# Optimization experiments

Measured on AMD Instinct MI355X. Metric: run time of the kernel, lower is better.

## Reference

```python
import jax, jax.numpy as jnp
import numpy as np

N_HEAD = 12


def build_mask(T, N):
    """Boolean mask, True = blocked. Mirrors st_mask construction for
    text_mask_mode='none', domain_present=None, text_to_motion_attn=False."""
    L = 3 * T + 5 * N
    r = jnp.arange(T)
    causal = r[:, None] >= r[None, :]          # allowed (lower-tri incl diag)
    strict = r[:, None] > r[None, :]           # allowed (strictly lower)
    m = jnp.zeros((L, L), dtype=bool)
    ml = 3 * T
    # motion-motion region starts fully blocked, then 7 sub-blocks opened
    m = m.at[:ml, :ml].set(True)
    m = m.at[0:T, 0:T].set(~causal)
    m = m.at[T:2 * T, 0:T].set(~causal)
    m = m.at[T:2 * T, T:2 * T].set(~strict)
    m = m.at[T:2 * T, 2 * T:3 * T].set(~strict)
    m = m.at[2 * T:3 * T, 0:T].set(~causal)
    m = m.at[2 * T:3 * T, T:2 * T].set(~causal)
    m = m.at[2 * T:3 * T, 2 * T:3 * T].set(~strict)
    # motion queries -> text keys: blocked by default
    m = m.at[:ml, ml:].set(True)
    # text queries -> motion keys: blocked (text_to_motion_attn=False)
    m = m.at[ml:, :ml].set(True)
    # text_mask_mode='none': up/down motion rows attend ALL text domains
    m = m.at[T:3 * T, ml:].set(False)
    return m


def setup_inputs() -> dict:
    key = jax.random.key(0)
    ks = jax.random.split(key, 9)
    C = 768
    B, T, N = 4, 512, 16
    L = 3 * T + 5 * N
    s = 1.0 / np.sqrt(C)
    return {
        "x": jax.random.normal(ks[0], (B, L, C), dtype=jnp.float32),
        "Wq": jax.random.normal(ks[1], (C, C), dtype=jnp.float32) * s,
        "bq": jax.random.normal(ks[2], (C,), dtype=jnp.float32) * 0.02,
        "Wk": jax.random.normal(ks[3], (C, C), dtype=jnp.float32) * s,
        "bk": jax.random.normal(ks[4], (C,), dtype=jnp.float32) * 0.02,
        "Wv": jax.random.normal(ks[5], (C, C), dtype=jnp.float32) * s,
        "bv": jax.random.normal(ks[6], (C,), dtype=jnp.float32) * 0.02,
        "Wp": jax.random.normal(ks[7], (C, C), dtype=jnp.float32) * s,
        "bp": jax.random.normal(ks[8], (C,), dtype=jnp.float32) * 0.02,
        "T_motion": 512,
        "N": 16,
    }


def reference(x, Wq, bq, Wk, bk, Wv, bv, Wp, bp, T_motion, N):
    B, L, C = x.shape
    nh = N_HEAD
    hd = C // nh
    # projections (torch Linear: x @ W.T + b)
    q = (x @ Wq.T + bq).reshape(B, L, nh, hd).transpose(0, 2, 1, 3)
    k = (x @ Wk.T + bk).reshape(B, L, nh, hd).transpose(0, 2, 1, 3)
    v = (x @ Wv.T + bv).reshape(B, L, nh, hd).transpose(0, 2, 1, 3)
    att = jnp.einsum('bhqd,bhkd->bhqk', q, k) * (1.0 / np.sqrt(hd))
    mask = build_mask(T_motion, N)                 # [L, L], True = blocked
    att = jnp.where(mask[None, None], -jnp.inf, att)
    att = jax.nn.softmax(att, axis=-1)
    y = jnp.einsum('bhqk,bhkd->bhqd', att, v)      # [B, nh, L, hd]
    y = y.transpose(0, 2, 1, 3).reshape(B, L, C)
    return y @ Wp.T + bp
```

## Files before the change

### kernel.cpp

```cpp
#include <hip/hip_runtime.h>

typedef _Float16 half8_t __attribute__((ext_vector_type(8)));
typedef _Float16 half4_t __attribute__((ext_vector_type(4)));
typedef int      int2_t  __attribute__((ext_vector_type(2)));
typedef float    f32x4   __attribute__((ext_vector_type(4)));

#define L_TOT 1616
#define L_PAD 1664
#define ML    1536
#define TT    512
#define CDIM  768
#define HD    64
#define NH    12
#define MTOT  6464

#define QK_SCALE 0.1803368801f
#define FIXED_M 10.0f

#if __has_builtin(__builtin_amdgcn_exp2f)
#define EXP2F(x) __builtin_amdgcn_exp2f(x)
#else
#define EXP2F(x) __expf((x) * 0.69314718056f)
#endif

typedef __attribute__((address_space(3))) void  as3_void;
typedef const __attribute__((address_space(1))) void as1_void;
__device__ __forceinline__ void gload_lds16(const void* g, void* l) {
  __builtin_amdgcn_global_load_lds((as1_void*)g, (as3_void*)l, 16, 0, 0);
}

__device__ __forceinline__ bool is_blocked(int i, int j) {
  if (j >= L_TOT) return true;
  if (i >= ML) return j < ML;
  if (j >= ML) return i < TT;
  int bi = i >> 9, bj = j >> 9;
  int a = i & 511, c = j & 511;
  if (bi == 0) return !(bj == 0 && c <= a);
  if (bi == 1) {
    if (bj == 0) return !(c <= a);
    return !(c < a);
  }
  if (bj == 2) return !(c < a);
  return !(c <= a);
}

__device__ __forceinline__ void mask_interval(int qrow, int k0, int& lo, int& hi) {
  lo = 0; hi = L_TOT - 1;
  if (qrow >= L_TOT)      { hi = -1; }
  else if (qrow >= ML)    { lo = ML; }
  else if (k0 >= ML)      { }
  else {
    int bi = qrow >> 9, bj = k0 >> 9, a = qrow & 511;
    if (bi == 0 && bj > 0) hi = -1;
    else {
      int strict = (bj > 0 && !(bi == 2 && bj == 1)) ? 1 : 0;
      hi = bj * 512 + a - strict;
    }
  }
}

__global__ __launch_bounds__(256) void cvt_kernel(
    const float* __restrict__ x, const float* __restrict__ wq,
    const float* __restrict__ wk, const float* __restrict__ wv,
    const float* __restrict__ wp, _Float16* __restrict__ Xh,
    _Float16* __restrict__ Wh)
{
  const int XN = MTOT * CDIM, WN = CDIM * CDIM;
  int i = (blockIdx.x * 256 + threadIdx.x) * 4;
  const float* src; _Float16* dst;
  if (i < XN) { src = x + i; dst = Xh + i; }
  else {
    int off = i - XN;
    int which = off / WN, rem = off - which * WN;
    const float* w = (which == 0) ? wq : (which == 1) ? wk : (which == 2) ? wv : wp;
    src = w + rem; dst = Wh + off;
  }
  float4 f = *(const float4*)src;
  half4_t h;
  h[0] = (_Float16)f.x; h[1] = (_Float16)f.y;
  h[2] = (_Float16)f.z; h[3] = (_Float16)f.w;
  *(half4_t*)dst = h;
}

__global__ __launch_bounds__(256) void gemm128_kernel(
    const _Float16* __restrict__ A, const _Float16* __restrict__ W,
    const float* __restrict__ bq, const float* __restrict__ bk,
    const float* __restrict__ bv, const float* __restrict__ bp,
    _Float16* __restrict__ Qh, _Float16* __restrict__ Kh,
    _Float16* __restrict__ Vt, float* __restrict__ Out, int fused)
{
  __shared__ __align__(16) _Float16 As[128 * 64];
  __shared__ __align__(16) _Float16 Bs[128 * 64];
  int stcols = fused ? 3 : 1;
  int id = blockIdx.x;
  int st = id / 48, local = id - st * 48;
  int band = st / stcols, stc = st - band * stcols;
  int tm = band * 8 + (local & 7);
  int tn = stc * 6 + (local >> 3);
  if (tm >= 51) return;
  int tid = threadIdx.x;
  int w = tid >> 6, lane = tid & 63;
  int wm = w & 1, wn = w >> 1;
  int lr = lane & 15, quad = lane >> 4;
  f32x4 acc[4][4];
#pragma unroll
  for (int i = 0; i < 4; i++)
#pragma unroll
    for (int j = 0; j < 4; j++) acc[i][j] = (f32x4){0.f, 0.f, 0.f, 0.f};
  int glog = ((lane & 7) ^ (lane >> 3)) * 8;
  const _Float16* gA[4]; const _Float16* gB[4];
#pragma unroll
  for (int u = 0; u < 4; u++) {
    int rl = (w * 4 + u) * 8 + (lane >> 3);
    int ar = tm * 128 + rl; if (ar >= MTOT) ar = MTOT - 1;
    gA[u] = A + (size_t)ar * CDIM + glog;
    gB[u] = W + (size_t)(tn * 128 + rl) * CDIM + glog;
  }
  const int lsw = lr & 7;
  for (int k0 = 0; k0 < CDIM; k0 += 64) {
    __syncthreads();
#pragma unroll
    for (int u = 0; u < 4; u++) {
      gload_lds16(gA[u] + k0, As + (w * 4 + u) * 512);
      gload_lds16(gB[u] + k0, Bs + (w * 4 + u) * 512);
    }
    __syncthreads();
#pragma unroll
    for (int kg = 0; kg < 8; kg += 4) {
      half8_t a[4], b[4];
#pragma unroll
      for (int g = 0; g < 4; g++) {
        a[g] = *(const half8_t*)(As + (wm * 64 + g * 16 + lr) * 64 + (((quad + kg) ^ lsw) * 8));
        b[g] = *(const half8_t*)(Bs + (wn * 64 + g * 16 + lr) * 64 + (((quad + kg) ^ lsw) * 8));
      }
#pragma unroll
      for (int mg = 0; mg < 4; mg++)
#pragma unroll
        for (int ng = 0; ng < 4; ng++)
          acc[mg][ng] = __builtin_amdgcn_mfma_f32_16x16x32_f16(a[mg], b[ng],
                                                               acc[mg][ng], 0, 0, 0);
    }
  }
  int mat, cbase;
  const float* bias;
  if (fused) { mat = tn / 6; cbase = (tn % 6) * 128;
               bias = (mat == 0) ? bq : (mat == 1) ? bk : bv; }
  else       { mat = 3; cbase = tn * 128; bias = bp; }
#pragma unroll
  for (int mg = 0; mg < 4; mg++) {
#pragma unroll
    for (int ng = 0; ng < 4; ng++) {
      int colt = wn * 64 + ng * 16 + lr;
      int c = cbase + colt;
      float bval = bias[c];
      int h = c >> 6, d = c & 63;
      int m0 = tm * 128 + wm * 64 + mg * 16 + quad * 4;
      if (mat == 3) {
        for (int r = 0; r < 4; r++) {
          int m = m0 + r;
          if (m < MTOT) Out[(size_t)m * CDIM + c] = acc[mg][ng][r] + bval;
        }
      } else if (mat == 2) {
        if (m0 < MTOT) {
          int b = m0 / L_TOT, l0 = m0 - b * L_TOT;
          int l0p = (l0 & ~63) | ((((l0 >> 2) & 3) << 4) | (((l0 >> 4) & 3) << 2));
          half4_t hv;
          for (int r = 0; r < 4; r++) hv[r] = (_Float16)(acc[mg][ng][r] + bval);
          *(half4_t*)&Vt[((size_t)(b * NH + h) * HD + d) * L_PAD + l0p] = hv;
        }
      } else {
        _Float16* dst = (mat == 0) ? Qh : Kh;
        for (int r = 0; r < 4; r++) {
          int m = m0 + r;
          if (m < MTOT) {
            int b = m / L_TOT, l = m - b * L_TOT;
            dst[((size_t)(b * NH + h) * L_PAD + l) * HD + d] = (_Float16)(acc[mg][ng][r] + bval);
          }
        }
      }
    }
  }
}

__global__ __launch_bounds__(256) void attn_kernel(
    const _Float16* __restrict__ Qh, const _Float16* __restrict__ Kh,
    const _Float16* __restrict__ Vt, _Float16* __restrict__ Yh)
{
  __shared__ __align__(16) _Float16 smem[16384];
  int qx = blockIdx.x;
  int qt = (qx < 24) ? (23 - qx) : qx;
  int bh = blockIdx.y;
  int b = bh / NH, h = bh - b * NH;
  const _Float16* Qb = Qh + (size_t)bh * L_PAD * HD;
  const _Float16* Kb = Kh + (size_t)bh * L_PAD * HD;
  const _Float16* Vb = Vt + (size_t)bh * HD * L_PAD;
  int tid = threadIdx.x;
  int w = tid >> 6, lane = tid & 63;
  int lr = lane & 15, quad = lane >> 4;
  const int lsw = lr & 7;

  int qrow = qt * 64 + w * 16 + lr;
  half8_t qf0 = *(const half8_t*)(Qb + (size_t)qrow * HD + quad * 8);
  half8_t qf1 = *(const half8_t*)(Qb + (size_t)qrow * HD + 32 + quad * 8);
  {
    _Float16 sc = (_Float16)QK_SCALE;
#pragma unroll
    for (int j = 0; j < 8; j++) { qf0[j] *= sc; qf1[j] *= sc; }
  }

  float l_run = 0.f;
  f32x4 oacc[4];
  for (int mt = 0; mt < 4; mt++) oacc[mt] = (f32x4){0.f, 0.f, 0.f, 0.f};

  int glog = ((lane & 7) ^ (lane >> 3)) * 8;
  const _Float16* pK[2]; const _Float16* pV[2];
#pragma unroll
  for (int u = 0; u < 2; u++) {
    int rl = (w * 2 + u) * 8 + (lane >> 3);
    pK[u] = Kb + (size_t)rl * HD + glog;
    pV[u] = Vb + (size_t)rl * L_PAD + glog;
  }
  int dmaOff0 = (w * 2) * 512, dmaOff1 = (w * 2 + 1) * 512;
  const int kOff0 = lr * 64 + (quad ^ lsw) * 8;
  const int kOff1 = lr * 64 + (((quad + 4) & 7) ^ lsw) * 8;
  const int vOff0 = lr * 64 + ((2 * quad) ^ lsw) * 8;
  const int vOff1 = lr * 64 + ((2 * quad + 1) ^ lsw) * 8;

  int i_max = qt * 64 + 63; if (i_max >= L_TOT) i_max = L_TOT - 1;
  int i_min = qt * 64;

  auto issue = [&](int kt, int buf) {
    int k0 = kt * 64;
    _Float16* kb = smem + buf * 4096;
    _Float16* vb = smem + 8192 + buf * 4096;
    gload_lds16(pK[0] + ((size_t)k0 << 6), kb + dmaOff0);
    gload_lds16(pK[1] + ((size_t)k0 << 6), kb + dmaOff1);
    gload_lds16(pV[0] + k0, vb + dmaOff0);
    gload_lds16(pV[1] + k0, vb + dmaOff1);
  };

  int kt_cur = 0;
  while (is_blocked(i_max, kt_cur * 64)) kt_cur++;
  int cur = 0;
  issue(kt_cur, 0);
  for (;;) {
    int kn = kt_cur + 1;
    while (kn < 26 && is_blocked(i_max, kn * 64)) kn++;
    bool has_next = (kn < 26);
    if (has_next) {
      issue(kn, cur ^ 1);
      asm volatile("s_waitcnt vmcnt(4)" ::: "memory");
    } else {
      asm volatile("s_waitcnt vmcnt(0)" ::: "memory");
    }
    asm volatile("s_barrier" ::: "memory");
    {
      int k0 = kt_cur * 64;
      bool full = (kt_cur != 25) && !is_blocked(i_min, k0 + 63);
      const _Float16* kb = smem + cur * 4096;
      const _Float16* vb = smem + 8192 + cur * 4096;
      f32x4 s4[4];
#pragma unroll
      for (int cg = 0; cg < 4; cg++) {
        half8_t kf0 = *(const half8_t*)(kb + kOff0 + cg * 1024);
        half8_t kf1 = *(const half8_t*)(kb + kOff1 + cg * 1024);
        f32x4 z = (f32x4){0.f, 0.f, 0.f, 0.f};
        z = __builtin_amdgcn_mfma_f32_16x16x32_f16(kf0, qf0, z, 0, 0, 0);
        z = __builtin_amdgcn_mfma_f32_16x16x32_f16(kf1, qf1, z, 0, 0, 0);
        s4[cg] = z;
      }
      if (!full) {
        int lo, hi;
        mask_interval(qrow, k0, lo, hi);
#pragma unroll
        for (int cg = 0; cg < 4; cg++) {
          int kbs = k0 + cg * 16 + quad * 4;
#pragma unroll
          for (int r = 0; r < 4; r++) {
            int j = kbs + r;
            if (j < lo || j > hi) s4[cg][r] = -1e30f;
          }
        }
      }
      int packed[8];
      float ladd = 0.f;
#pragma unroll
      for (int cg = 0; cg < 4; cg++) {
        float p0 = EXP2F(s4[cg][0] - FIXED_M);
        float p1 = EXP2F(s4[cg][1] - FIXED_M);
        float p2 = EXP2F(s4[cg][2] - FIXED_M);
        float p3 = EXP2F(s4[cg][3] - FIXED_M);
        ladd += (p0 + p1) + (p2 + p3);
        packed[cg * 2]     = __builtin_bit_cast(int, __builtin_amdgcn_cvt_pkrtz(p0, p1));
        packed[cg * 2 + 1] = __builtin_bit_cast(int, __builtin_amdgcn_cvt_pkrtz(p2, p3));
      }
      l_run += ladd;
#pragma unroll
      for (int p = 0; p < 2; p++) {
        const _Float16* vbp = vb + (p ? vOff1 : vOff0);
        int2_t piL; piL[0] = packed[(2 * p) * 2];     piL[1] = packed[(2 * p) * 2 + 1];
        int2_t piH; piH[0] = packed[(2 * p + 1) * 2]; piH[1] = packed[(2 * p + 1) * 2 + 1];
        half4_t pbL = __builtin_bit_cast(half4_t, piL);
        half4_t pbH = __builtin_bit_cast(half4_t, piH);
#pragma unroll
        for (int mt2 = 0; mt2 < 4; mt2++) {
          half8_t v8 = *(const half8_t*)(vbp + mt2 * 1024);
          half4_t vlo = __builtin_shufflevector(v8, v8, 0, 1, 2, 3);
          half4_t vhi = __builtin_shufflevector(v8, v8, 4, 5, 6, 7);
          oacc[mt2] = __builtin_amdgcn_mfma_f32_16x16x16f16(vlo, pbL, oacc[mt2], 0, 0, 0);
          oacc[mt2] = __builtin_amdgcn_mfma_f32_16x16x16f16(vhi, pbH, oacc[mt2], 0, 0, 0);
        }
      }
    }
    if (!has_next) break;
    asm volatile("s_barrier" ::: "memory");
    kt_cur = kn; cur ^= 1;
  }
  l_run += __shfl_xor(l_run, 16);
  l_run += __shfl_xor(l_run, 32);
  __syncthreads();
  _Float16* Os = smem;
  float inv = 1.f / l_run;
#pragma unroll
  for (int mt2 = 0; mt2 < 4; mt2++)
    for (int r = 0; r < 4; r++)
      Os[(w * 16 + lr) * 72 + mt2 * 16 + quad * 4 + r] =
          (_Float16)(oacc[mt2][r] * inv);
  __syncthreads();
  {
    int rr = w * 16 + (lane >> 2);
    int cc = (lane & 3) * 16;
    int i = qt * 64 + rr;
    if (i < L_TOT) {
      const _Float16* srcp = Os + rr * 72 + cc;
      int4 y0 = *(const int4*)srcp;
      int4 y1 = *(const int4*)(srcp + 8);
      _Float16* dst = Yh + ((size_t)(b * L_TOT) + i) * CDIM + h * HD + cc;
      *(int4*)dst = y0;
      *(int4*)(dst + 8) = y1;
    }
  }
}

extern "C" void kernel_launch(void* const* d_in, const int* in_sizes, int n_in,
                              void* d_out, int out_size, void* d_ws, size_t ws_size,
                              hipStream_t stream)
{
  const float* x  = (const float*)d_in[0];
  const float* Wq = (const float*)d_in[1];
  const float* bq = (const float*)d_in[2];
  const float* Wk = (const float*)d_in[3];
  const float* bk = (const float*)d_in[4];
  const float* Wv = (const float*)d_in[5];
  const float* bv = (const float*)d_in[6];
  const float* Wp = (const float*)d_in[7];
  const float* bp = (const float*)d_in[8];
  float* out = (float*)d_out;

  _Float16* ws = (_Float16*)d_ws;
  const size_t XN  = (size_t)MTOT * CDIM;
  const size_t WN  = (size_t)CDIM * CDIM;
  const size_t XNP = (size_t)48 * L_PAD * HD;
  _Float16* Xh = ws;
  _Float16* Wh = Xh + XN;
  _Float16* Qh = Wh + 4 * WN;
  _Float16* Kh = Qh + XNP;
  _Float16* Vt = Kh + XNP;
  _Float16* Yh = Xh;

  const int cvt_blocks = (int)((XN + 4 * WN) / 4 / 256);
  cvt_kernel<<<cvt_blocks, 256, 0, stream>>>(x, Wq, Wk, Wv, Wp, Xh, Wh);
  gemm128_kernel<<<dim3(1008), 256, 0, stream>>>(Xh, Wh, bq, bk, bv, bp,
                                                 Qh, Kh, Vt, out, 1);
  attn_kernel<<<dim3(26, 48), 256, 0, stream>>>(Qh, Kh, Vt, Yh);
  gemm128_kernel<<<dim3(336), 256, 0, stream>>>(Yh, Wh + 3 * WN, bq, bk, bv, bp,
                                                Qh, Kh, Vt, out, 0);
}
```

Baseline: 206.0 us.

## Double-buffer GEMM LDS tiles with k32 stages and async prefetch

The projection GEMM moves from a single 128x64 LDS tile per k-step to double-buffered 128x32 tiles. The next stage's global-to-LDS loads are issued before computing on the current buffer, using explicit vmcnt waits and raw s_barrier. This aims to overlap global memory latency with MFMA work, at the cost of twice as many barrier rounds and a new XOR swizzle for the 32-wide rows.

```diff
diff --git a/kernel.cpp b/kernel.cpp
--- a/kernel.cpp
+++ b/kernel.cpp
@@ -89,8 +89,8 @@
     _Float16* __restrict__ Qh, _Float16* __restrict__ Kh,
     _Float16* __restrict__ Vt, float* __restrict__ Out, int fused)
 {
-  __shared__ __align__(16) _Float16 As[128 * 64];
-  __shared__ __align__(16) _Float16 Bs[128 * 64];
+  __shared__ __align__(16) _Float16 As[2 * 4096];
+  __shared__ __align__(16) _Float16 Bs[2 * 4096];
   int stcols = fused ? 3 : 1;
   int id = blockIdx.x;
   int st = id / 48, local = id - st * 48;
@@ -107,39 +107,59 @@
   for (int i = 0; i < 4; i++)
 #pragma unroll
     for (int j = 0; j < 4; j++) acc[i][j] = (f32x4){0.f, 0.f, 0.f, 0.f};
-  int glog = ((lane & 7) ^ (lane >> 3)) * 8;
-  const _Float16* gA[4]; const _Float16* gB[4];
-#pragma unroll
-  for (int u = 0; u < 4; u++) {
-    int rl = (w * 4 + u) * 8 + (lane >> 3);
+  int ric = lane >> 2;
+  int glog = ((lane & 3) ^ (ric & 3) ^ ((lane >> 4) & 3)) * 8;
+  const _Float16* gA[2]; const _Float16* gB[2];
+  int ldsOff[2];
+#pragma unroll
+  for (int u = 0; u < 2; u++) {
+    int c = w * 2 + u;
+    int rl = c * 16 + ric;
     int ar = tm * 128 + rl; if (ar >= MTOT) ar = MTOT - 1;
     gA[u] = A + (size_t)ar * CDIM + glog;
     gB[u] = W + (size_t)(tn * 128 + rl) * CDIM + glog;
-  }
-  const int lsw = lr & 7;
-  for (int k0 = 0; k0 < CDIM; k0 += 64) {
-    __syncthreads();
-#pragma unroll
-    for (int u = 0; u < 4; u++) {
-      gload_lds16(gA[u] + k0, As + (w * 4 + u) * 512);
-      gload_lds16(gB[u] + k0, Bs + (w * 4 + u) * 512);
-    }
-    __syncthreads();
-#pragma unroll
-    for (int kg = 0; kg < 8; kg += 4) {
-      half8_t a[4], b[4];
-#pragma unroll
-      for (int g = 0; g < 4; g++) {
-        a[g] = *(const half8_t*)(As + (wm * 64 + g * 16 + lr) * 64 + (((quad + kg) ^ lsw) * 8));
-        b[g] = *(const half8_t*)(Bs + (wn * 64 + g * 16 + lr) * 64 + (((quad + kg) ^ lsw) * 8));
-      }
-#pragma unroll
-      for (int mg = 0; mg < 4; mg++)
-#pragma unroll
-        for (int ng = 0; ng < 4; ng++)
-          acc[mg][ng] = __builtin_amdgcn_mfma_f32_16x16x32_f16(a[mg], b[ng],
-                                                               acc[mg][ng], 0, 0, 0);
-    }
+    ldsOff[u] = c * 512;
+  }
+  const int pg = (quad ^ (lr & 3) ^ ((lr >> 2) & 3)) * 8;
+  const int aBase = (wm * 64 + lr) * 32 + pg;
+  const int bBase = (wn * 64 + lr) * 32 + pg;
+
+#define GEMM_ISSUE(s, buf)                                        \
+  {                                                               \
+    int k0_ = (s) * 32;                                           \
+    _Float16* ab = As + (buf) * 4096;                             \
+    _Float16* bb = Bs + (buf) * 4096;                             \
+    gload_lds16(gA[0] + k0_, ab + ldsOff[0]);                     \
+    gload_lds16(gA[1] + k0_, ab + ldsOff[1]);                     \
+    gload_lds16(gB[0] + k0_, bb + ldsOff[0]);                     \
+    gload_lds16(gB[1] + k0_, bb + ldsOff[1]);                     \
+  }
+
+  GEMM_ISSUE(0, 0)
+  for (int s = 0; s < 24; s++) {
+    int cur = s & 1;
+    if (s < 23) {
+      GEMM_ISSUE(s + 1, cur ^ 1)
+      asm volatile("s_waitcnt vmcnt(4)" ::: "memory");
+    } else {
+      asm volatile("s_waitcnt vmcnt(0)" ::: "memory");
+    }
+    asm volatile("s_barrier" ::: "memory");
+    const _Float16* as = As + cur * 4096;
+    const _Float16* bs = Bs + cur * 4096;
+    half8_t a[4], b[4];
+#pragma unroll
+    for (int g = 0; g < 4; g++) {
+      a[g] = *(const half8_t*)(as + aBase + g * 512);
+      b[g] = *(const half8_t*)(bs + bBase + g * 512);
+    }
+#pragma unroll
+    for (int mg = 0; mg < 4; mg++)
+#pragma unroll
+      for (int ng = 0; ng < 4; ng++)
+        acc[mg][ng] = __builtin_amdgcn_mfma_f32_16x16x32_f16(a[mg], b[ng],
+                                                             acc[mg][ng], 0, 0, 0);
+    if (s < 23) asm volatile("s_barrier" ::: "memory");
   }
   int mat, cbase;
   const float* bias;
@@ -180,6 +200,7 @@
       }
     }
   }
+#undef GEMM_ISSUE
 }
 
 __global__ __launch_bounds__(256) void attn_kernel(
```

Measured after the change: 218.2 us. 1.06x slower.
